# Performance work log

Measured on AMD Instinct MI355X. Metric: run time of the kernel, lower is better.

## Reference

```python
import jax, jax.numpy as jnp
import numpy as np

TAU = 2.0      # spikingjelly LIFNode default tau
VTH = 1.0      # default v_threshold
ALPHA = 4.0    # default surrogate.Sigmoid alpha
EPS = 1e-5     # BatchNorm eps


@jax.custom_vjp
def spike(x):
    # Heaviside with sigmoid surrogate gradient (spikingjelly default)
    return (x >= 0.0).astype(x.dtype)

def _spike_fwd(x):
    return spike(x), x

def _spike_bwd(x, g):
    sg = jax.nn.sigmoid(ALPHA * x)
    return (g * ALPHA * sg * (1.0 - sg),)

spike.defvjp(_spike_fwd, _spike_bwd)


def lif(x_seq):
    """Multi-step LIF over leading time dim. x_seq: [T, B, C, H, W].
    decay_input=True, v_reset=0.0 (hard reset), detach_reset=True."""
    def step(v, x):
        v = v + (x - v) / TAU                     # charge
        s = spike(v - VTH)                        # fire
        v = v * (1.0 - jax.lax.stop_gradient(s))  # hard reset to 0, detached
        return v, s
    _, s_seq = jax.lax.scan(step, jnp.zeros_like(x_seq[0]), x_seq)
    return s_seq


def bn(x, gamma, beta, mean, var):
    # inference-mode BatchNorm2d over channel dim C of [T, B, C, H, W]
    inv = gamma * jax.lax.rsqrt(var + EPS)
    return x * inv[:, None, None] + (beta - mean * inv)[:, None, None]


def setup_inputs() -> dict:
    key = jax.random.key(0)
    ks = jax.random.split(key, 8)
    T, B, C, H, W = 4, 32, 512, 14, 14
    Ch = 4 * C
    inp = jax.random.normal(ks[0], (T, B, C, H, W), dtype=jnp.float32)
    W1 = jax.random.normal(ks[1], (Ch, C), dtype=jnp.float32) / np.sqrt(C)
    W2 = jax.random.normal(ks[2], (C, Ch), dtype=jnp.float32) / np.sqrt(Ch)
    gamma1 = jnp.ones((Ch,), jnp.float32)
    beta1 = jnp.zeros((Ch,), jnp.float32)
    mean1 = 0.1 * jax.random.normal(ks[3], (Ch,), dtype=jnp.float32)
    var1 = jax.random.uniform(ks[4], (Ch,), jnp.float32, 0.5, 1.5)
    gamma2 = jnp.ones((C,), jnp.float32)
    beta2 = jnp.zeros((C,), jnp.float32)
    mean2 = 0.1 * jax.random.normal(ks[5], (C,), dtype=jnp.float32)
    var2 = jax.random.uniform(ks[6], (C,), jnp.float32, 0.5, 1.5)
    return {"input": inp, "W1": W1, "gamma1": gamma1, "beta1": beta1,
            "mean1": mean1, "var1": var1, "W2": W2, "gamma2": gamma2,
            "beta2": beta2, "mean2": mean2, "var2": var2}


def reference(input, W1, gamma1, beta1, mean1, var1, W2, gamma2, beta2, mean2, var2):
    s1 = lif(input)                                  # [T,B,C,H,W] spikes
    h = jnp.einsum('tbchw,oc->tbohw', s1, W1)        # 1x1 conv, no bias
    h = bn(h, gamma1, beta1, mean1, var1)
    s2 = lif(h)                                      # [T,B,4C,H,W] spikes
    y = jnp.einsum('tbchw,oc->tbohw', s2, W2)        # 1x1 conv, no bias
    y = bn(y, gamma2, beta2, mean2, var2)
    return y + input                                 # residual
```

## Files before the change

kernel.cpp:

```cpp
#include <hip/hip_runtime.h>
#include <stdint.h>


typedef __bf16 bf16x8 __attribute__((ext_vector_type(8)));
typedef _Float16 f16x8 __attribute__((ext_vector_type(8)));
typedef float f32x4 __attribute__((ext_vector_type(4)));
typedef int i32x4 __attribute__((ext_vector_type(4)));

#define TPLANE 3211264u
#define NCOL   6272u
#define MFMA_F16 __builtin_amdgcn_mfma_f32_16x16x32_f16
#define MFMA_I8  __builtin_amdgcn_mfma_i32_16x16x64_i8

static __device__ __forceinline__ void async16(const void* g, void* l) {
  __builtin_amdgcn_global_load_lds((const __attribute__((address_space(1))) uint32_t*)g,
                                   (__attribute__((address_space(3))) uint32_t*)l, 16, 0, 0);
}

__global__ void prep_kernel(const float* __restrict__ W1,
                            const float* __restrict__ g1, const float* __restrict__ b1,
                            const float* __restrict__ m1, const float* __restrict__ v1,
                            _Float16* __restrict__ W1h,
                            float* __restrict__ scale1, float* __restrict__ bias1) {
  uint32_t i = blockIdx.x * 512u + threadIdx.x;
  W1h[i] = (_Float16)W1[i];
  if (i < 2048u) { float s = g1[i] / sqrtf(v1[i] + 1e-5f); scale1[i] = s; bias1[i] = b1[i] - m1[i] * s; }
}

__global__ void prep2_kernel(const float* __restrict__ W2,
                             const float* __restrict__ g2, const float* __restrict__ b2,
                             const float* __restrict__ m2, const float* __restrict__ v2,
                             signed char* __restrict__ W2q,
                             float* __restrict__ scale2, float* __restrict__ bias2) {
  __shared__ float red[256];
  const uint32_t c = blockIdx.x, tid = threadIdx.x;
  const float* row = W2 + (size_t)c * 2048u;
  float vals[8];
  float mx = 0.f;
  #pragma unroll
  for (int j = 0; j < 8; ++j) {
    vals[j] = row[tid + 256u * (uint32_t)j];
    mx = fmaxf(mx, fabsf(vals[j]));
  }
  red[tid] = mx; __syncthreads();
  for (uint32_t s = 128u; s > 0u; s >>= 1) {
    if (tid < s) red[tid] = fmaxf(red[tid], red[tid + s]);
    __syncthreads();
  }
  const float rmax = red[0];
  const float inv = rmax > 0.f ? 127.f / rmax : 0.f;
  #pragma unroll
  for (int j = 0; j < 8; ++j)
    W2q[(size_t)c * 2048u + tid + 256u * (uint32_t)j] =
        (signed char)__float2int_rn(vals[j] * inv);
  if (tid == 0) {
    float bn = g2[c] / sqrtf(v2[c] + 1e-5f);
    scale2[c] = (rmax / 127.f) * bn;
    bias2[c]  = b2[c] - m2[c] * bn;
  }
}

__global__ void lif1_kernel(const float* __restrict__ x, uint16_t* __restrict__ s1) {
  __shared__ __align__(16) uint16_t sl[64 * 66 * 4];
  const uint32_t tid = threadIdx.x;
  const uint32_t c0 = blockIdx.x * 64u;
  const uint32_t n0 = blockIdx.y * 64u;
  #pragma unroll
  for (int j = 0; j < 16; ++j) {
    uint32_t idx = (uint32_t)j * 256u + tid;
    uint32_t cl = idx >> 6, nl = idx & 63u;
    uint32_t n = n0 + nl;
    uint32_t b = n / 196u, hw = n - b * 196u;
    const float* px = x + (size_t)(b * 512u + c0 + cl) * 196u + hw;
    float v = 0.f;
    uint16_t sp[4];
    #pragma unroll
    for (int t = 0; t < 4; ++t) {
      float xv = px[(size_t)t * TPLANE];
      v += (xv - v) * 0.5f;
      bool s = (v >= 1.0f);
      sp[t] = s ? (uint16_t)0x3C00u : (uint16_t)0u;
      v = s ? 0.f : v;
    }
    uint2 pk;
    pk.x = (uint32_t)sp[0] | ((uint32_t)sp[1] << 16);
    pk.y = (uint32_t)sp[2] | ((uint32_t)sp[3] << 16);
    *(uint2*)&sl[(cl * 66u + nl) * 4u] = pk;
  }
  __syncthreads();
  #pragma unroll
  for (int j = 0; j < 8; ++j) {
    uint32_t id = (uint32_t)j * 256u + tid;
    uint32_t nl = id & 63u, t = (id >> 6) & 3u, cb = id >> 8;
    uint32_t us[4];
    #pragma unroll
    for (int e = 0; e < 4; ++e) {
      uint32_t lo16 = sl[((cb * 8u + 2u * e) * 66u + nl) * 4u + t];
      uint32_t hi16 = sl[((cb * 8u + 2u * e + 1u) * 66u + nl) * 4u + t];
      us[e] = lo16 | (hi16 << 16);
    }
    uint32_t chunk = (((c0 >> 3) + cb) * 4u + t) * NCOL + n0 + nl;
    uint4 o4; o4.x = us[0]; o4.y = us[1]; o4.z = us[2]; o4.w = us[3];
    *(uint4*)(s1 + (size_t)chunk * 8u) = o4;
  }
}

__launch_bounds__(512)
__global__ void gemm1_lif2_kernel(const _Float16* __restrict__ W1h,
                                  const uint16_t* __restrict__ s1,
                                  const float* __restrict__ scale1,
                                  const float* __restrict__ bias1,
                                  signed char* __restrict__ s2) {
  __shared__ __align__(16) char lds[49152];
  char* ldsA = lds;
  char* ldsB = lds + 16384;
  const uint32_t tid = threadIdx.x;
  const uint32_t wid = tid >> 6;
  const uint32_t lane = tid & 63u;
  const uint32_t il = lane & 15u, g = lane >> 4;
  const uint32_t wm = wid >> 2, wn = wid & 3u;
  const uint32_t bid = blockIdx.x;
  const uint32_t lid = (bid & 7u) * 196u + (bid >> 3);
  const uint32_t m0 = (lid & 15u) * 128u;
  const uint32_t n0 = (lid >> 4) * 64u;

  f32x4 acc[4][4];
  #pragma unroll
  for (int i = 0; i < 4; ++i)
    #pragma unroll
    for (int j = 0; j < 4; ++j) acc[i][j] = (f32x4){0.f, 0.f, 0.f, 0.f};

  for (int kt = 0; kt < 8; ++kt) {
    const uint32_t k0 = (uint32_t)kt * 64u;
    #pragma unroll
    for (uint32_t r = 0; r < 2; ++r) {
      uint32_t cid = r * 512u + tid;
      uint32_t i = cid >> 3, q = cid & 7u;
      const char* src = (const char*)W1h + (size_t)(m0 + i) * 1024u + (size_t)k0 * 2u
                        + (size_t)((q ^ (i & 7u)) * 16u);
      async16(src, ldsA + (r * 512u + wid * 64u) * 16u);
    }
    #pragma unroll
    for (uint32_t r = 0; r < 4; ++r) {
      uint32_t cid = r * 512u + tid;
      uint32_t kb = cid >> 8, rem = cid & 255u;
      uint32_t tt = rem >> 6, dn = rem & 63u;
      const char* src = (const char*)s1
          + (size_t)((((k0 >> 3) + kb) * 4u + tt) * NCOL + n0 + dn) * 16u;
      async16(src, ldsB + (r * 512u + wid * 64u) * 16u);
    }
    __syncthreads();
    #pragma unroll
    for (int ks = 0; ks < 2; ++ks) {
      f16x8 af[4], bfr0, bfr1;
      #pragma unroll
      for (int th = 0; th < 2; ++th) {
        #pragma unroll
        for (int fm = 0; fm < 4; ++fm) {
          uint32_t i = wm * 64u + (uint32_t)fm * 16u + il;
          uint32_t q = (uint32_t)ks * 4u + g;
          af[fm] = *(const f16x8*)(ldsA + (i * 8u + (q ^ (i & 7u))) * 16u);
        }
        uint32_t ch = g * 4096u + wn * 1024u + il * 16u
                      + (uint32_t)th * 512u + (uint32_t)ks * 16384u;
        bfr0 = *(const f16x8*)(ldsB + ch);
        bfr1 = *(const f16x8*)(ldsB + ch + 256u);
        #pragma unroll
        for (int fm = 0; fm < 4; ++fm) {
          acc[fm][th*2]   = MFMA_F16(af[fm], bfr0, acc[fm][th*2], 0, 0, 0);
          acc[fm][th*2+1] = MFMA_F16(af[fm], bfr1, acc[fm][th*2+1], 0, 0, 0);
        }
      }
    }
    __syncthreads();
  }

  const uint32_t n = n0 + wn * 16u + il;
  #pragma unroll
  for (int fm = 0; fm < 4; ++fm) {
    const uint32_t ch0 = m0 + wm * 64u + (uint32_t)fm * 16u + 4u * g;
    f32x4 sc = *(const f32x4*)&scale1[ch0];
    f32x4 bi = *(const f32x4*)&bias1[ch0];
    float v0 = 0.f, v1 = 0.f, v2 = 0.f, v3 = 0.f;
    #pragma unroll
    for (int t = 0; t < 4; ++t) {
      float h0 = acc[fm][t][0] * sc[0] + bi[0];
      float h1 = acc[fm][t][1] * sc[1] + bi[1];
      float h2 = acc[fm][t][2] * sc[2] + bi[2];
      float h3 = acc[fm][t][3] * sc[3] + bi[3];
      v0 += (h0 - v0) * 0.5f; bool s0 = (v0 >= 1.0f); v0 = s0 ? 0.f : v0;
      v1 += (h1 - v1) * 0.5f; bool s1v = (v1 >= 1.0f); v1 = s1v ? 0.f : v1;
      v2 += (h2 - v2) * 0.5f; bool s2v = (v2 >= 1.0f); v2 = s2v ? 0.f : v2;
      v3 += (h3 - v3) * 0.5f; bool s3v = (v3 >= 1.0f); v3 = s3v ? 0.f : v3;
      uint32_t pk = (s0 ? 1u : 0u) | (s1v ? 0x100u : 0u)
                  | (s2v ? 0x10000u : 0u) | (s3v ? 0x1000000u : 0u);
      uint32_t chunk = ((ch0 >> 4) * 4u + (uint32_t)t) * NCOL + n;
      *(uint32_t*)((char*)s2 + (size_t)chunk * 16u + (size_t)(ch0 & 15u)) = pk;
    }
  }
}

__launch_bounds__(512)
__global__ void gemm2_out_kernel(const signed char* __restrict__ W2q,
                                 const signed char* __restrict__ s2,
                                 const float* __restrict__ scale2,
                                 const float* __restrict__ bias2,
                                 const float* __restrict__ xin,
                                 float* __restrict__ outp) {
  __shared__ __align__(16) char lds[49152];
  char* ldsA = lds;
  char* ldsB = lds + 16384;
  float* ep = (float*)lds;
  const uint32_t tid = threadIdx.x;
  const uint32_t wid = tid >> 6;
  const uint32_t lane = tid & 63u;
  const uint32_t il = lane & 15u, g = lane >> 4;
  const uint32_t wm = wid >> 2, wn = wid & 3u;
  const uint32_t bid = blockIdx.x;
  const uint32_t lid = (bid & 7u) * 49u + (bid >> 3);
  const uint32_t m0 = (lid & 3u) * 128u;
  const uint32_t n0 = (lid >> 2) * 64u;

  i32x4 acc[4][4];
  #pragma unroll
  for (int i = 0; i < 4; ++i)
    #pragma unroll
    for (int j = 0; j < 4; ++j) acc[i][j] = (i32x4){0, 0, 0, 0};

  for (int kt = 0; kt < 16; ++kt) {
    #pragma unroll
    for (uint32_t r = 0; r < 4; ++r) {
      uint32_t cid = r * 512u + tid;
      uint32_t kb = cid >> 8, rem = cid & 255u;
      uint32_t tt = rem >> 6, dn = rem & 63u;
      const char* src = (const char*)s2
          + (size_t)((((uint32_t)kt * 8u + kb) * 4u + tt) * NCOL + n0 + dn) * 16u;
      async16(src, ldsB + (size_t)cid * 16u);
    }
    #pragma unroll
    for (uint32_t r = 0; r < 2; ++r) {
      uint32_t cid = r * 512u + tid;
      uint32_t i = cid >> 3, q = cid & 7u;
      const char* src = (const char*)W2q + (size_t)(m0 + i) * 2048u
                        + (size_t)((uint32_t)kt * 128u) + (size_t)((q ^ (i & 7u)) * 16u);
      async16(src, ldsA + (size_t)cid * 16u);
    }
    __syncthreads();
    #pragma unroll
    for (int ks = 0; ks < 2; ++ks) {
      i32x4 af[4], bfr0, bfr1;
      #pragma unroll
      for (int fm = 0; fm < 4; ++fm) {
        uint32_t i = wm * 64u + (uint32_t)fm * 16u + il;
        uint32_t q = (uint32_t)ks * 4u + g;
        af[fm] = *(const i32x4*)(ldsA + (i * 8u + (q ^ (i & 7u))) * 16u);
      }
      #pragma unroll
      for (int th = 0; th < 2; ++th) {
        uint32_t chb = ((((uint32_t)ks * 4u + g) * 4u + (uint32_t)th * 2u) * 64u
                        + wn * 16u + il) * 16u;
        bfr0 = *(const i32x4*)(ldsB + chb);
        bfr1 = *(const i32x4*)(ldsB + chb + 1024u);
        #pragma unroll
        for (int fm = 0; fm < 4; ++fm) {
          acc[fm][th*2]   = MFMA_I8(af[fm], bfr0, acc[fm][th*2], 0, 0, 0);
          acc[fm][th*2+1] = MFMA_I8(af[fm], bfr1, acc[fm][th*2+1], 0, 0, 0);
        }
      }
    }
    __syncthreads();
  }

  const uint32_t cl = lane >> 2, qq = lane & 3u;
  #pragma unroll
  for (int fm = 0; fm < 4; ++fm) {
    const uint32_t cbase = m0 + wm * 64u + (uint32_t)fm * 16u;
    f32x4 sc = *(const f32x4*)&scale2[cbase + 4u * g];
    f32x4 bi = *(const f32x4*)&bias2[cbase + 4u * g];
    #pragma unroll
    for (int t = 0; t < 4; ++t)
      #pragma unroll
      for (int r = 0; r < 4; ++r)
        ep[wid * 1280u + ((4u * g + (uint32_t)r) * 4u + (uint32_t)t) * 20u + il]
            = (float)acc[fm][t][r] * sc[r] + bi[r];
    __syncthreads();
    #pragma unroll
    for (int t = 0; t < 4; ++t) {
      f32x4 val = *(const f32x4*)&ep[wid * 1280u + (cl * 4u + (uint32_t)t) * 20u + qq * 4u];
      uint32_t nn = n0 + wn * 16u + qq * 4u;
      uint32_t b = nn / 196u, hw = nn - b * 196u;
      uint32_t c = cbase + cl;
      size_t off = (((size_t)t * 32u + b) * 512u + c) * 196u + hw;
      f32x4 iv = *(const f32x4*)(xin + off);
      *(f32x4*)(outp + off) = val + iv;
    }
    __syncthreads();
  }
}

extern "C" void kernel_launch(void* const* d_in, const int* in_sizes, int n_in,
                              void* d_out, int out_size, void* d_ws, size_t ws_size,
                              hipStream_t stream) {
  const float* x  = (const float*)d_in[0];
  const float* W1 = (const float*)d_in[1];
  const float* g1 = (const float*)d_in[2];
  const float* b1 = (const float*)d_in[3];
  const float* m1 = (const float*)d_in[4];
  const float* v1 = (const float*)d_in[5];
  const float* W2 = (const float*)d_in[6];
  const float* g2 = (const float*)d_in[7];
  const float* b2 = (const float*)d_in[8];
  const float* m2 = (const float*)d_in[9];
  const float* v2 = (const float*)d_in[10];
  float* out = (float*)d_out;
  char* ws = (char*)d_ws;

  signed char* s2b    = (signed char*)(ws);
  uint16_t*    s1b    = (uint16_t*)(ws + 102760448);
  _Float16*    W1h    = (_Float16*)(ws + 128450560);
  signed char* W2q    = (signed char*)(ws + 132644864);
  float*       scale1 = (float*)(ws + 134742016);
  float*       bias1  = (float*)(ws + 134750208);
  float*       scale2 = (float*)(ws + 134758400);
  float*       bias2  = (float*)(ws + 134760448);

  prep_kernel<<<2048, 512, 0, stream>>>(W1, g1, b1, m1, v1, W1h, scale1, bias1);
  prep2_kernel<<<512, 256, 0, stream>>>(W2, g2, b2, m2, v2, W2q, scale2, bias2);
  lif1_kernel<<<dim3(8, 98), 256, 0, stream>>>(x, s1b);
  gemm1_lif2_kernel<<<1568, 512, 0, stream>>>(W1h, s1b, scale1, bias1, s2b);
  gemm2_out_kernel<<<392, 512, 0, stream>>>(W2q, s2b, scale2, bias2, x, out);
}
```

Baseline: 126.8 us.

## Quantize W1 to int8 and run first GEMM with int8 MFMA on int8 spikes

W1 is now quantized per output row to int8 with a scale folded into the BN scale, and layer-1 spikes are stored as int8 bytes instead of fp16. The first GEMM switches from f16 MFMA to i32 int8 MFMA, which halves the K-loop iterations and the bytes moved for both operands. Per-row int8 rounding of W1 can flip spikes near the threshold, so the output is only approximate.

```diff
diff --git a/kernel.cpp b/kernel.cpp
--- a/kernel.cpp
+++ b/kernel.cpp
@@ -2,29 +2,42 @@
 #include <stdint.h>
 
 
-typedef __bf16 bf16x8 __attribute__((ext_vector_type(8)));
-typedef _Float16 f16x8 __attribute__((ext_vector_type(8)));
 typedef float f32x4 __attribute__((ext_vector_type(4)));
 typedef int i32x4 __attribute__((ext_vector_type(4)));
 
 #define TPLANE 3211264u
 #define NCOL   6272u
-#define MFMA_F16 __builtin_amdgcn_mfma_f32_16x16x32_f16
-#define MFMA_I8  __builtin_amdgcn_mfma_i32_16x16x64_i8
+#define MFMA_I8 __builtin_amdgcn_mfma_i32_16x16x64_i8
 
 static __device__ __forceinline__ void async16(const void* g, void* l) {
   __builtin_amdgcn_global_load_lds((const __attribute__((address_space(1))) uint32_t*)g,
                                    (__attribute__((address_space(3))) uint32_t*)l, 16, 0, 0);
 }
 
-__global__ void prep_kernel(const float* __restrict__ W1,
-                            const float* __restrict__ g1, const float* __restrict__ b1,
-                            const float* __restrict__ m1, const float* __restrict__ v1,
-                            _Float16* __restrict__ W1h,
-                            float* __restrict__ scale1, float* __restrict__ bias1) {
-  uint32_t i = blockIdx.x * 512u + threadIdx.x;
-  W1h[i] = (_Float16)W1[i];
-  if (i < 2048u) { float s = g1[i] / sqrtf(v1[i] + 1e-5f); scale1[i] = s; bias1[i] = b1[i] - m1[i] * s; }
+__global__ void prep1_kernel(const float* __restrict__ W1,
+                             const float* __restrict__ g1, const float* __restrict__ b1,
+                             const float* __restrict__ m1, const float* __restrict__ v1,
+                             signed char* __restrict__ W1q,
+                             float* __restrict__ scale1, float* __restrict__ bias1) {
+  __shared__ float red[256];
+  const uint32_t c = blockIdx.x, tid = threadIdx.x;
+  const float* row = W1 + (size_t)c * 512u;
+  float v0 = row[tid], v1l = row[tid + 256u];
+  float mx = fmaxf(fabsf(v0), fabsf(v1l));
+  red[tid] = mx; __syncthreads();
+  for (uint32_t s = 128u; s > 0u; s >>= 1) {
+    if (tid < s) red[tid] = fmaxf(red[tid], red[tid + s]);
+    __syncthreads();
+  }
+  const float rmax = red[0];
+  const float inv = rmax > 0.f ? 127.f / rmax : 0.f;
+  W1q[(size_t)c * 512u + tid]        = (signed char)__float2int_rn(v0 * inv);
+  W1q[(size_t)c * 512u + tid + 256u] = (signed char)__float2int_rn(v1l * inv);
+  if (tid == 0) {
+    float bn = g1[c] / sqrtf(v1[c] + 1e-5f);
+    scale1[c] = (rmax / 127.f) * bn;
+    bias1[c]  = b1[c] - m1[c] * bn;
+  }
 }
 
 __global__ void prep2_kernel(const float* __restrict__ W2,
@@ -60,7 +73,7 @@
   }
 }
 
-__global__ void lif1_kernel(const float* __restrict__ x, uint16_t* __restrict__ s1) {
+__global__ void lif1_kernel(const float* __restrict__ x, signed char* __restrict__ s1) {
   __shared__ __align__(16) uint16_t sl[64 * 66 * 4];
   const uint32_t tid = threadIdx.x;
   const uint32_t c0 = blockIdx.x * 64u;
@@ -79,7 +92,7 @@
       float xv = px[(size_t)t * TPLANE];
       v += (xv - v) * 0.5f;
       bool s = (v >= 1.0f);
-      sp[t] = s ? (uint16_t)0x3C00u : (uint16_t)0u;
+      sp[t] = s ? (uint16_t)1u : (uint16_t)0u;
       v = s ? 0.f : v;
     }
     uint2 pk;
@@ -89,25 +102,27 @@
   }
   __syncthreads();
   #pragma unroll
-  for (int j = 0; j < 8; ++j) {
+  for (int j = 0; j < 4; ++j) {
     uint32_t id = (uint32_t)j * 256u + tid;
     uint32_t nl = id & 63u, t = (id >> 6) & 3u, cb = id >> 8;
     uint32_t us[4];
     #pragma unroll
-    for (int e = 0; e < 4; ++e) {
-      uint32_t lo16 = sl[((cb * 8u + 2u * e) * 66u + nl) * 4u + t];
-      uint32_t hi16 = sl[((cb * 8u + 2u * e + 1u) * 66u + nl) * 4u + t];
-      us[e] = lo16 | (hi16 << 16);
-    }
-    uint32_t chunk = (((c0 >> 3) + cb) * 4u + t) * NCOL + n0 + nl;
+    for (int w = 0; w < 4; ++w) {
+      uint32_t b0 = sl[((cb * 16u + (uint32_t)w * 4u + 0u) * 66u + nl) * 4u + t];
+      uint32_t b1 = sl[((cb * 16u + (uint32_t)w * 4u + 1u) * 66u + nl) * 4u + t];
+      uint32_t b2 = sl[((cb * 16u + (uint32_t)w * 4u + 2u) * 66u + nl) * 4u + t];
+      uint32_t b3 = sl[((cb * 16u + (uint32_t)w * 4u + 3u) * 66u + nl) * 4u + t];
+      us[w] = b0 | (b1 << 8) | (b2 << 16) | (b3 << 24);
+    }
+    uint32_t chunk = (((c0 >> 4) + cb) * 4u + t) * NCOL + n0 + nl;
     uint4 o4; o4.x = us[0]; o4.y = us[1]; o4.z = us[2]; o4.w = us[3];
-    *(uint4*)(s1 + (size_t)chunk * 8u) = o4;
+    *(uint4*)(s1 + (size_t)chunk * 16u) = o4;
   }
 }
 
 __launch_bounds__(512)
-__global__ void gemm1_lif2_kernel(const _Float16* __restrict__ W1h,
-                                  const uint16_t* __restrict__ s1,
+__global__ void gemm1_lif2_kernel(const signed char* __restrict__ W1q,
+                                  const signed char* __restrict__ s1,
                                   const float* __restrict__ scale1,
                                   const float* __restrict__ bias1,
                                   signed char* __restrict__ s2) {
@@ -124,51 +139,50 @@
   const uint32_t m0 = (lid & 15u) * 128u;
   const uint32_t n0 = (lid >> 4) * 64u;
 
-  f32x4 acc[4][4];
+  i32x4 acc[4][4];
   #pragma unroll
   for (int i = 0; i < 4; ++i)
     #pragma unroll
-    for (int j = 0; j < 4; ++j) acc[i][j] = (f32x4){0.f, 0.f, 0.f, 0.f};
-
-  for (int kt = 0; kt < 8; ++kt) {
-    const uint32_t k0 = (uint32_t)kt * 64u;
-    #pragma unroll
-    for (uint32_t r = 0; r < 2; ++r) {
-      uint32_t cid = r * 512u + tid;
-      uint32_t i = cid >> 3, q = cid & 7u;
-      const char* src = (const char*)W1h + (size_t)(m0 + i) * 1024u + (size_t)k0 * 2u
-                        + (size_t)((q ^ (i & 7u)) * 16u);
-      async16(src, ldsA + (r * 512u + wid * 64u) * 16u);
-    }
+    for (int j = 0; j < 4; ++j) acc[i][j] = (i32x4){0, 0, 0, 0};
+
+  for (int kt = 0; kt < 4; ++kt) {
     #pragma unroll
     for (uint32_t r = 0; r < 4; ++r) {
       uint32_t cid = r * 512u + tid;
       uint32_t kb = cid >> 8, rem = cid & 255u;
       uint32_t tt = rem >> 6, dn = rem & 63u;
       const char* src = (const char*)s1
-          + (size_t)((((k0 >> 3) + kb) * 4u + tt) * NCOL + n0 + dn) * 16u;
-      async16(src, ldsB + (r * 512u + wid * 64u) * 16u);
+          + (size_t)((((uint32_t)kt * 8u + kb) * 4u + tt) * NCOL + n0 + dn) * 16u;
+      async16(src, ldsB + (size_t)cid * 16u);
+    }
+    #pragma unroll
+    for (uint32_t r = 0; r < 2; ++r) {
+      uint32_t cid = r * 512u + tid;
+      uint32_t i = cid >> 3, q = cid & 7u;
+      const char* src = (const char*)W1q + (size_t)(m0 + i) * 512u
+                        + (size_t)((uint32_t)kt * 128u) + (size_t)((q ^ (i & 7u)) * 16u);
+      async16(src, ldsA + (size_t)cid * 16u);
     }
     __syncthreads();
     #pragma unroll
     for (int ks = 0; ks < 2; ++ks) {
-      f16x8 af[4], bfr0, bfr1;
+      i32x4 af[4], bfr0, bfr1;
+      #pragma unroll
+      for (int fm = 0; fm < 4; ++fm) {
+        uint32_t i = wm * 64u + (uint32_t)fm * 16u + il;
+        uint32_t q = (uint32_t)ks * 4u + g;
+        af[fm] = *(const i32x4*)(ldsA + (i * 8u + (q ^ (i & 7u))) * 16u);
+      }
       #pragma unroll
       for (int th = 0; th < 2; ++th) {
+        uint32_t chb = ((((uint32_t)ks * 4u + g) * 4u + (uint32_t)th * 2u) * 64u
+                        + wn * 16u + il) * 16u;
+        bfr0 = *(const i32x4*)(ldsB + chb);
+        bfr1 = *(const i32x4*)(ldsB + chb + 1024u);
         #pragma unroll
         for (int fm = 0; fm < 4; ++fm) {
-          uint32_t i = wm * 64u + (uint32_t)fm * 16u + il;
-          uint32_t q = (uint32_t)ks * 4u + g;
-          af[fm] = *(const f16x8*)(ldsA + (i * 8u + (q ^ (i & 7u))) * 16u);
-        }
-        uint32_t ch = g * 4096u + wn * 1024u + il * 16u
-                      + (uint32_t)th * 512u + (uint32_t)ks * 16384u;
-        bfr0 = *(const f16x8*)(ldsB + ch);
-        bfr1 = *(const f16x8*)(ldsB + ch + 256u);
-        #pragma unroll
-        for (int fm = 0; fm < 4; ++fm) {
-          acc[fm][th*2]   = MFMA_F16(af[fm], bfr0, acc[fm][th*2], 0, 0, 0);
-          acc[fm][th*2+1] = MFMA_F16(af[fm], bfr1, acc[fm][th*2+1], 0, 0, 0);
+          acc[fm][th*2]   = MFMA_I8(af[fm], bfr0, acc[fm][th*2], 0, 0, 0);
+          acc[fm][th*2+1] = MFMA_I8(af[fm], bfr1, acc[fm][th*2+1], 0, 0, 0);
         }
       }
     }
@@ -184,10 +198,10 @@
     float v0 = 0.f, v1 = 0.f, v2 = 0.f, v3 = 0.f;
     #pragma unroll
     for (int t = 0; t < 4; ++t) {
-      float h0 = acc[fm][t][0] * sc[0] + bi[0];
-      float h1 = acc[fm][t][1] * sc[1] + bi[1];
-      float h2 = acc[fm][t][2] * sc[2] + bi[2];
-      float h3 = acc[fm][t][3] * sc[3] + bi[3];
+      float h0 = (float)acc[fm][t][0] * sc[0] + bi[0];
+      float h1 = (float)acc[fm][t][1] * sc[1] + bi[1];
+      float h2 = (float)acc[fm][t][2] * sc[2] + bi[2];
+      float h3 = (float)acc[fm][t][3] * sc[3] + bi[3];
       v0 += (h0 - v0) * 0.5f; bool s0 = (v0 >= 1.0f); v0 = s0 ? 0.f : v0;
       v1 += (h1 - v1) * 0.5f; bool s1v = (v1 >= 1.0f); v1 = s1v ? 0.f : v1;
       v2 += (h2 - v2) * 0.5f; bool s2v = (v2 >= 1.0f); v2 = s2v ? 0.f : v2;
@@ -316,17 +330,17 @@
   char* ws = (char*)d_ws;
 
   signed char* s2b    = (signed char*)(ws);
-  uint16_t*    s1b    = (uint16_t*)(ws + 102760448);
-  _Float16*    W1h    = (_Float16*)(ws + 128450560);
+  signed char* s1b    = (signed char*)(ws + 102760448);
+  signed char* W1q    = (signed char*)(ws + 128450560);
   signed char* W2q    = (signed char*)(ws + 132644864);
   float*       scale1 = (float*)(ws + 134742016);
   float*       bias1  = (float*)(ws + 134750208);
   float*       scale2 = (float*)(ws + 134758400);
   float*       bias2  = (float*)(ws + 134760448);
 
-  prep_kernel<<<2048, 512, 0, stream>>>(W1, g1, b1, m1, v1, W1h, scale1, bias1);
+  prep1_kernel<<<2048, 256, 0, stream>>>(W1, g1, b1, m1, v1, W1q, scale1, bias1);
   prep2_kernel<<<512, 256, 0, stream>>>(W2, g2, b2, m2, v2, W2q, scale2, bias2);
   lif1_kernel<<<dim3(8, 98), 256, 0, stream>>>(x, s1b);
-  gemm1_lif2_kernel<<<1568, 512, 0, stream>>>(W1h, s1b, scale1, bias1, s2b);
+  gemm1_lif2_kernel<<<1568, 512, 0, stream>>>(W1q, s1b, scale1, bias1, s2b);
   gemm2_out_kernel<<<392, 512, 0, stream>>>(W2q, s2b, scale2, bias2, x, out);
 }
```

Result: faster. 104.6 us (median of 2 runs) (-17.5%).
